# Kernel optimization log

Measured on AMD Instinct MI355X. Metric: run time of the kernel, lower is better.

## Reference

```python
import jax, jax.numpy as jnp
import numpy as np
from jax import lax

B = 32768  # number of 5x5 patches processed in a batch
NUM_MID = 6  # middle 25->25 conv layers (layers 1..6 of 8)
NUM_W = 6    # predicted kernel weights per pixel


def _conv(x, w, b, pad):
    # x: [B,C,H,W], w: [O,I,kh,kw]
    y = lax.conv_general_dilated(x, w, (1, 1), pad,
                                 dimension_numbers=('NCHW', 'OIHW', 'NCHW'))
    return y + b[None, :, None, None]


def setup_inputs() -> dict:
    key = jax.random.key(0)
    ks = jax.random.split(key, 10)
    s = 0.1
    inp = {
        'input': jax.random.normal(ks[0], (B, 8, 5, 5), dtype=jnp.float32),
        'w0': jax.random.normal(ks[1], (25, 8, 3, 3), dtype=jnp.float32) * s,
        'b0': jax.random.normal(ks[2], (25,), dtype=jnp.float32) * s,
        'wmid': jax.random.normal(ks[3], (NUM_MID, 25, 25, 3, 3), dtype=jnp.float32) * s,
        'bmid': jax.random.normal(ks[4], (NUM_MID, 25), dtype=jnp.float32) * s,
        'wlast': jax.random.normal(ks[5], (NUM_W, 25, 3, 3), dtype=jnp.float32) * s,
        'blast': jax.random.normal(ks[6], (NUM_W,), dtype=jnp.float32) * s,
        'wpost': jax.random.normal(ks[7], (3 * NUM_W, 3, 5, 5), dtype=jnp.float32) * s,
        'bpost': jax.random.normal(ks[8], (3 * NUM_W,), dtype=jnp.float32) * s,
    }
    return inp


def reference(input, w0, b0, wmid, bmid, wlast, blast, wpost, bpost):
    # 8-layer tiny CNN predicting per-pixel softmax weights over NUM_W kernels
    h = jax.nn.relu(_conv(input, w0, b0, 'SAME'))
    for i in range(NUM_MID):  # fixed small layer count
        h = jax.nn.relu(_conv(h, wmid[i], bmid[i], 'SAME'))
    h = _conv(h, wlast, blast, 'SAME')            # [B, NUM_W, 5, 5]
    norm_w = jax.nn.softmax(h, axis=1)            # softmax over weight channels
    # postconv: 5x5 valid conv on first 3 channels -> [B, 3*NUM_W, 1, 1] -> [B,3,NUM_W]
    colors = _conv(input[:, 0:3], wpost, bpost, 'VALID').reshape(B, 3, NUM_W)
    # per-pixel matmul: filtered[:,y,x] = colors @ norm_w[:,y,x]
    filtered = jnp.einsum('bcw,bwyx->bcyx', colors, norm_w)  # [B,3,5,5]
    return filtered
```

## Files before the change

kernel.cpp:

```cpp
#include <hip/hip_runtime.h>
#include <hip/hip_bf16.h>
#include <stdint.h>


typedef short bf16x8 __attribute__((ext_vector_type(8)));
typedef float f32x4  __attribute__((ext_vector_type(4)));

#define WSB_N     73728
#define WSB_EMB   6144
#define WSF_BYTE  147456
#define WSF_BALL  0
#define WSF_BP32  256
#define WSF_N     1624

__device__ __forceinline__ float b2f(unsigned short u) {
  union { unsigned int u; float f; } v; v.u = ((unsigned int)u) << 16; return v.f;
}
__device__ __forceinline__ unsigned short f2b(float f) {
  union { float f; unsigned int u; } v; v.f = f;
  unsigned int r = v.u + 0x7fffu + ((v.u >> 16) & 1u);
  return (unsigned short)(r >> 16);
}
__device__ __forceinline__ unsigned int pk2(float lo, float hi) {
  __hip_bfloat162 h = __float22bfloat162_rn(make_float2(lo, hi));
  union { __hip_bfloat162 h; unsigned int u; } v; v.h = h; return v.u;
}
__device__ __forceinline__ bool sniff_is_f32(const void* w0raw) {
  const unsigned short* q = (const unsigned short*)w0raw;
  int hits = 0;
  #pragma unroll
  for (int i = 0; i < 64; ++i) {
    unsigned int e = (q[i] >> 7) & 0xFFu;
    if (e >= 130u) ++hits;
  }
  return hits > 0;
}
__device__ __forceinline__ float ldw(const void* p, long idx, bool f32) {
  return f32 ? ((const float*)p)[idx] : b2f(((const unsigned short*)p)[idx]);
}
__device__ __forceinline__ int kperm(int m) {
  return (m < 16) ? ((m >> 2) * 8 + (m & 3))
                  : (((m - 16) >> 2) * 8 + 4 + (m & 3));
}

__global__ void prep_weights(const void* __restrict__ w0,
                             const void* __restrict__ b0,
                             const void* __restrict__ wm,
                             const void* __restrict__ bm,
                             const void* __restrict__ wl,
                             const void* __restrict__ bl,
                             const void* __restrict__ wp,
                             const void* __restrict__ bp,
                             unsigned short* __restrict__ wsb,
                             float* __restrict__ wsf) {
  const bool f32 = sniff_is_f32(w0);
  int e = blockIdx.x * blockDim.x + threadIdx.x;
  if (e < WSB_N) {
    int l = e / 9216, r = e % 9216, t = r / 1024, r2 = r % 1024;
    int o = r2 >> 5, c = r2 & 31;
    if (l == 7 && o >= 6) return;
    float v = 0.f;
    if (l < 7) {
      int co = kperm(o);
      if (co < 25) {
        if (l == 0) { if (c < 8)  v = ldw(w0, (co * 8 + c) * 9 + t, f32); }
        else        { if (c < 25) v = ldw(wm, (((l - 1) * 25 + co) * 25 + c) * 9 + t, f32); }
      }
    } else {
      if (c < 25) v = ldw(wl, (o * 25 + c) * 9 + t, f32);
    }
    wsb[e] = f2b(v);
  } else if (e < WSB_N + WSB_EMB) {
    int idx = e - WSB_N;
    int hl = idx / 3072, rem = idx % 3072;
    int chunk = rem / 1024, r2 = rem % 1024;
    int o = r2 >> 5, k = r2 & 31;
    float w = (o < 18 && k < 25) ? ldw(wp, (o * 3 + chunk) * 25 + k, f32) : 0.f;
    unsigned short hi = f2b(w);
    unsigned short val = hl ? f2b(w - b2f(hi)) : hi;
    int rowidx = hl * 96 + chunk * 32 + o;
    int t = rowidx / 26, rr = 6 + rowidx % 26;
    wsb[7 * 9216 + t * 1024 + rr * 32 + k] = val;
  } else {
    int q = e - WSB_N - WSB_EMB;
    if (q < 256) {
      int l = q >> 5, m = q & 31;
      float v = 0.f;
      if (l < 7) {
        int co = kperm(m);
        if (co < 25) v = (l == 0) ? ldw(b0, co, f32) : ldw(bm, (l - 1) * 25 + co, f32);
      } else {
        if (m < 6) v = ldw(bl, m, f32);
      }
      wsf[WSF_BALL + q] = v;
    } else if (q < 288) {
      int oc = q - 256;
      wsf[WSF_BP32 + oc] = (oc < 18) ? ldw(bp, oc, f32) : 0.f;
    }
  }
}

__global__ __launch_bounds__(64)
__attribute__((amdgpu_waves_per_eu(2, 2)))
void pcnn_mfma(
    const void* __restrict__ inp,
    const void* __restrict__ w0raw,
    const unsigned short* __restrict__ wsb,
    const float* __restrict__ wsf,
    void* __restrict__ out) {
  __shared__ __align__(16) unsigned char pool[13696];
  short* stage = (short*)pool;
  short* inpk  = (short*)(pool + 6400);
  float* colb  = (float*)(pool + 12544);
  float* smb   = (float*)pool;

  const bool f32m = sniff_is_f32(w0raw);
  const int lane = threadIdx.x;
  const int col  = lane & 15;
  const int quad = lane >> 4;
  const long g   = blockIdx.x;

  bf16x8 WC[2][3][2];
  #pragma unroll
  for (int hl = 0; hl < 2; ++hl)
    #pragma unroll
    for (int ch = 0; ch < 3; ++ch)
      #pragma unroll
      for (int hf = 0; hf < 2; ++hf) {
        const int rowidx = hl * 96 + ch * 32 + hf * 16 + col;
        const int t = rowidx / 26, rr = 6 + rowidx % 26;
        WC[hl][ch][hf] = *(const bf16x8*)(wsb + 7 * 9216 + t * 1024 + rr * 32 + quad * 8);
      }
  f32x4 c0 = *(const f32x4*)(wsf + WSF_BP32 + quad * 4);
  f32x4 c1 = *(const f32x4*)(wsf + WSF_BP32 + 16 + quad * 4);

  for (int i = lane; i < 672; i += 64) {
    int s = 25 + i % 7, rest = i / 7;
    inpk[rest * 32 + s] = 0;
  }

  #pragma unroll 1
  for (int c0i = 0; c0i < 3200; c0i += 1600) {
    float v[25];
    #pragma unroll
    for (int j = 0; j < 25; ++j)
      v[j] = ldw(inp, g * 3200 + c0i + j * 64 + lane, f32m);
    #pragma unroll
    for (int j = 0; j < 25; ++j) {
      const int e = c0i + j * 64 + lane;
      int b = e / 200, r = e % 200, c = r / 25, px = r % 25;
      unsigned short hi = f2b(v[j]);
      stage[px * 128 + b * 8 + c] = hi;
      if (c < 3) {
        inpk[((0 * 3 + c) * 16 + b) * 32 + px] = hi;
        inpk[((1 * 3 + c) * 16 + b) * 32 + px] = f2b(v[j] - b2f(hi));
      }
    }
  }
  __asm__ volatile("s_waitcnt lgkmcnt(0)" ::: "memory");

  #pragma unroll
  for (int ch = 0; ch < 3; ++ch) {
    bf16x8 Bhi = *(const bf16x8*)(inpk + ((0 * 3 + ch) * 16 + col) * 32 + quad * 8);
    bf16x8 Blo = *(const bf16x8*)(inpk + ((1 * 3 + ch) * 16 + col) * 32 + quad * 8);
    c0 = __builtin_amdgcn_mfma_f32_16x16x32_bf16(WC[0][ch][0], Bhi, c0, 0, 0, 0);
    c0 = __builtin_amdgcn_mfma_f32_16x16x32_bf16(WC[0][ch][0], Blo, c0, 0, 0, 0);
    c0 = __builtin_amdgcn_mfma_f32_16x16x32_bf16(WC[1][ch][0], Bhi, c0, 0, 0, 0);
    c1 = __builtin_amdgcn_mfma_f32_16x16x32_bf16(WC[0][ch][1], Bhi, c1, 0, 0, 0);
    c1 = __builtin_amdgcn_mfma_f32_16x16x32_bf16(WC[0][ch][1], Blo, c1, 0, 0, 0);
    c1 = __builtin_amdgcn_mfma_f32_16x16x32_bf16(WC[1][ch][1], Bhi, c1, 0, 0, 0);
  }
  #pragma unroll
  for (int r = 0; r < 4; ++r) colb[col * 18 + quad * 4 + r] = c0[r];
  if (quad == 0) { colb[col * 18 + 16] = c1[0]; colb[col * 18 + 17] = c1[1]; }

  bf16x8 X[25], Y[25];
  #pragma unroll
  for (int p = 0; p < 25; ++p) {
    union { bf16x8 v; uint4 q4; } t;
    t.q4 = make_uint4(0u, 0u, 0u, 0u);
    if (quad == 0) t.q4 = *(const uint4*)(stage + p * 128 + col * 8);
    X[p] = t.v;
  }

  auto conv = [&](const bf16x8 (&in)[25], bf16x8 (&outp)[25], int l) {
    const unsigned short* WA = wsb + l * 9216;
    bf16x8 A0[9], A1[9];
    #pragma unroll
    for (int t = 0; t < 9; ++t) {
      A0[t] = *(const bf16x8*)(WA + t * 1024 + col * 32 + quad * 8);
      A1[t] = *(const bf16x8*)(WA + t * 1024 + (16 + col) * 32 + quad * 8);
    }
    const f32x4 bias0 = *(const f32x4*)(wsf + WSF_BALL + l * 32 + quad * 4);
    const f32x4 bias1 = *(const f32x4*)(wsf + WSF_BALL + l * 32 + 16 + quad * 4);
    #pragma unroll
    for (int p = 0; p < 25; ++p) {
      const int py = p / 5, pxx = p % 5;
      f32x4 a0e = bias0, a1e = bias1;
      f32x4 a0o = {0.f, 0.f, 0.f, 0.f}, a1o = {0.f, 0.f, 0.f, 0.f};
      __builtin_amdgcn_s_setprio(1);
      #pragma unroll
      for (int dy = -1; dy <= 1; ++dy)
        #pragma unroll
        for (int dx = -1; dx <= 1; ++dx)
          if ((unsigned)(py + dy) < 5u && (unsigned)(pxx + dx) < 5u) {
            const int t = (dy + 1) * 3 + (dx + 1);
            const int q = p + dy * 5 + dx;
            if (t & 1) {
              a0o = __builtin_amdgcn_mfma_f32_16x16x32_bf16(A0[t], in[q], a0o, 0, 0, 0);
              a1o = __builtin_amdgcn_mfma_f32_16x16x32_bf16(A1[t], in[q], a1o, 0, 0, 0);
            } else {
              a0e = __builtin_amdgcn_mfma_f32_16x16x32_bf16(A0[t], in[q], a0e, 0, 0, 0);
              a1e = __builtin_amdgcn_mfma_f32_16x16x32_bf16(A1[t], in[q], a1e, 0, 0, 0);
            }
          }
      __builtin_amdgcn_s_setprio(0);
      union { bf16x8 v; unsigned int uu[4]; } nb;
      nb.uu[0] = pk2(fmaxf(a0e[0] + a0o[0], 0.f), fmaxf(a0e[1] + a0o[1], 0.f));
      nb.uu[1] = pk2(fmaxf(a0e[2] + a0o[2], 0.f), fmaxf(a0e[3] + a0o[3], 0.f));
      nb.uu[2] = pk2(fmaxf(a1e[0] + a1o[0], 0.f), fmaxf(a1e[1] + a1o[1], 0.f));
      nb.uu[3] = pk2(fmaxf(a1e[2] + a1o[2], 0.f), fmaxf(a1e[3] + a1o[3], 0.f));
      outp[p] = nb.v;
    }
  };

  conv(X, Y, 0);
  #pragma unroll 1
  for (int i = 0; i < 3; ++i) {
    conv(Y, X, 2 * i + 1);
    conv(X, Y, 2 * i + 2);
  }

  {
    const unsigned short* WA = wsb + 7 * 9216;
    bf16x8 A[9];
    #pragma unroll
    for (int t = 0; t < 9; ++t)
      A[t] = *(const bf16x8*)(WA + t * 1024 + col * 32 + quad * 8);
    const f32x4 biasl = *(const f32x4*)(wsf + WSF_BALL + 7 * 32 + quad * 4);
    #pragma unroll
    for (int p = 0; p < 25; ++p) {
      const int py = p / 5, pxx = p % 5;
      f32x4 ae = biasl, ao = {0.f, 0.f, 0.f, 0.f};
      __builtin_amdgcn_s_setprio(1);
      #pragma unroll
      for (int dy = -1; dy <= 1; ++dy)
        #pragma unroll
        for (int dx = -1; dx <= 1; ++dx)
          if ((unsigned)(py + dy) < 5u && (unsigned)(pxx + dx) < 5u) {
            const int t = (dy + 1) * 3 + (dx + 1);
            const int q = p + dy * 5 + dx;
            if (t & 1)
              ao = __builtin_amdgcn_mfma_f32_16x16x32_bf16(A[t], Y[q], ao, 0, 0, 0);
            else
              ae = __builtin_amdgcn_mfma_f32_16x16x32_bf16(A[t], Y[q], ae, 0, 0, 0);
          }
      __builtin_amdgcn_s_setprio(0);
      f32x4 a;
      a[0] = ae[0] + ao[0]; a[1] = ae[1] + ao[1];
      a[2] = ae[2] + ao[2]; a[3] = ae[3] + ao[3];
      float l4 = __shfl_xor(a[0], 16);
      float l5 = __shfl_xor(a[1], 16);
      if (quad == 0) {
        float m = fmaxf(fmaxf(fmaxf(a[0], a[1]), fmaxf(a[2], a[3])), fmaxf(l4, l5));
        float e0 = __expf(a[0] - m), e1 = __expf(a[1] - m), e2 = __expf(a[2] - m);
        float e3 = __expf(a[3] - m), e4 = __expf(l4 - m), e5 = __expf(l5 - m);
        float inv = 1.f / (e0 + e1 + e2 + e3 + e4 + e5);
        float* sp = smb + p * 96 + col * 6;
        sp[0] = e0 * inv; sp[1] = e1 * inv; sp[2] = e2 * inv;
        sp[3] = e3 * inv; sp[4] = e4 * inv; sp[5] = e5 * inv;
      }
    }
  }
  __asm__ volatile("s_waitcnt lgkmcnt(0)" ::: "memory");

  for (int e = lane; e < 1200; e += 64) {
    int b = e / 75, r = e % 75, c = r / 25, p = r % 25;
    float v = 0.f;
    #pragma unroll
    for (int w = 0; w < 6; ++w)
      v = fmaf(colb[b * 18 + c * 6 + w], smb[p * 96 + b * 6 + w], v);
    const long oidx = g * 1200 + e;
    if (f32m) ((float*)out)[oidx] = v;
    else      ((unsigned short*)out)[oidx] = f2b(v);
  }
}

extern "C" void kernel_launch(void* const* d_in, const int* in_sizes, int n_in,
                              void* d_out, int out_size, void* d_ws, size_t ws_size,
                              hipStream_t stream) {
  unsigned short* wsb = (unsigned short*)d_ws;
  float* wsf = (float*)((char*)d_ws + WSF_BYTE);
  const int B = in_sizes[0] / 200;

  const int prep_n = WSB_N + WSB_EMB + 288;
  prep_weights<<<(prep_n + 255) / 256, 256, 0, stream>>>(
      d_in[1], d_in[2], d_in[3], d_in[4], d_in[5], d_in[6], d_in[7], d_in[8],
      wsb, wsf);
  pcnn_mfma<<<B / 16, 64, 0, stream>>>(d_in[0], d_in[1], wsb, wsf, d_out);
}
```

Baseline: 159.4 us.

## Software-pipeline conv epilogues behind next pixel's MFMAs and pad LDS strides

The per-pixel epilogue (bias add, ReLU, bf16 pack, and in the last layer the softmax) is delayed by one iteration, so it runs while the next pixel's MFMA chain is in flight instead of stalling on the accumulator results. Separately, the LDS staging stride and the softmax buffer stride are padded (128 to 136 shorts, 96 to 98 floats) to reduce bank conflicts, and the shared pool grows to match. The cost is extra live accumulator registers, which could add pressure under the fixed waves-per-EU setting.

```diff
diff --git a/kernel.cpp b/kernel.cpp
--- a/kernel.cpp
+++ b/kernel.cpp
@@ -11,7 +11,12 @@
 #define WSF_BYTE  147456
 #define WSF_BALL  0
 #define WSF_BP32  256
-#define WSF_N     1624
+
+#define L_STAGE_STRIDE 136
+#define L_INPK   6800
+#define L_COLB   12944
+#define L_POOL   14096
+#define SMB_STRIDE 98
 
 __device__ __forceinline__ float b2f(unsigned short u) {
   union { unsigned int u; float f; } v; v.u = ((unsigned int)u) << 16; return v.f;
@@ -108,10 +113,10 @@
     const unsigned short* __restrict__ wsb,
     const float* __restrict__ wsf,
     void* __restrict__ out) {
-  __shared__ __align__(16) unsigned char pool[13696];
+  __shared__ __align__(16) unsigned char pool[L_POOL];
   short* stage = (short*)pool;
-  short* inpk  = (short*)(pool + 6400);
-  float* colb  = (float*)(pool + 12544);
+  short* inpk  = (short*)(pool + L_INPK);
+  float* colb  = (float*)(pool + L_COLB);
   float* smb   = (float*)pool;
 
   const bool f32m = sniff_is_f32(w0raw);
@@ -150,7 +155,7 @@
       const int e = c0i + j * 64 + lane;
       int b = e / 200, r = e % 200, c = r / 25, px = r % 25;
       unsigned short hi = f2b(v[j]);
-      stage[px * 128 + b * 8 + c] = hi;
+      stage[px * L_STAGE_STRIDE + b * 8 + c] = hi;
       if (c < 3) {
         inpk[((0 * 3 + c) * 16 + b) * 32 + px] = hi;
         inpk[((1 * 3 + c) * 16 + b) * 32 + px] = f2b(v[j] - b2f(hi));
@@ -179,7 +184,7 @@
   for (int p = 0; p < 25; ++p) {
     union { bf16x8 v; uint4 q4; } t;
     t.q4 = make_uint4(0u, 0u, 0u, 0u);
-    if (quad == 0) t.q4 = *(const uint4*)(stage + p * 128 + col * 8);
+    if (quad == 0) t.q4 = *(const uint4*)(stage + p * L_STAGE_STRIDE + col * 8);
     X[p] = t.v;
   }
 
@@ -193,6 +198,7 @@
     }
     const f32x4 bias0 = *(const f32x4*)(wsf + WSF_BALL + l * 32 + quad * 4);
     const f32x4 bias1 = *(const f32x4*)(wsf + WSF_BALL + l * 32 + 16 + quad * 4);
+    f32x4 p0e, p0o, p1e, p1o;
     #pragma unroll
     for (int p = 0; p < 25; ++p) {
       const int py = p / 5, pxx = p % 5;
@@ -215,12 +221,23 @@
             }
           }
       __builtin_amdgcn_s_setprio(0);
+      if (p > 0) {
+        union { bf16x8 v; unsigned int uu[4]; } nb;
+        nb.uu[0] = pk2(fmaxf(p0e[0] + p0o[0], 0.f), fmaxf(p0e[1] + p0o[1], 0.f));
+        nb.uu[1] = pk2(fmaxf(p0e[2] + p0o[2], 0.f), fmaxf(p0e[3] + p0o[3], 0.f));
+        nb.uu[2] = pk2(fmaxf(p1e[0] + p1o[0], 0.f), fmaxf(p1e[1] + p1o[1], 0.f));
+        nb.uu[3] = pk2(fmaxf(p1e[2] + p1o[2], 0.f), fmaxf(p1e[3] + p1o[3], 0.f));
+        outp[p - 1] = nb.v;
+      }
+      p0e = a0e; p0o = a0o; p1e = a1e; p1o = a1o;
+    }
+    {
       union { bf16x8 v; unsigned int uu[4]; } nb;
-      nb.uu[0] = pk2(fmaxf(a0e[0] + a0o[0], 0.f), fmaxf(a0e[1] + a0o[1], 0.f));
-      nb.uu[1] = pk2(fmaxf(a0e[2] + a0o[2], 0.f), fmaxf(a0e[3] + a0o[3], 0.f));
-      nb.uu[2] = pk2(fmaxf(a1e[0] + a1o[0], 0.f), fmaxf(a1e[1] + a1o[1], 0.f));
-      nb.uu[3] = pk2(fmaxf(a1e[2] + a1o[2], 0.f), fmaxf(a1e[3] + a1o[3], 0.f));
-      outp[p] = nb.v;
+      nb.uu[0] = pk2(fmaxf(p0e[0] + p0o[0], 0.f), fmaxf(p0e[1] + p0o[1], 0.f));
+      nb.uu[1] = pk2(fmaxf(p0e[2] + p0o[2], 0.f), fmaxf(p0e[3] + p0o[3], 0.f));
+      nb.uu[2] = pk2(fmaxf(p1e[0] + p1o[0], 0.f), fmaxf(p1e[1] + p1o[1], 0.f));
+      nb.uu[3] = pk2(fmaxf(p1e[2] + p1o[2], 0.f), fmaxf(p1e[3] + p1o[3], 0.f));
+      outp[24] = nb.v;
     }
   };
 
@@ -238,6 +255,20 @@
     for (int t = 0; t < 9; ++t)
       A[t] = *(const bf16x8*)(WA + t * 1024 + col * 32 + quad * 8);
     const f32x4 biasl = *(const f32x4*)(wsf + WSF_BALL + 7 * 32 + quad * 4);
+    f32x4 pa;
+    auto tail = [&](const f32x4& a, int p) {
+      float l4 = __shfl_xor(a[0], 16);
+      float l5 = __shfl_xor(a[1], 16);
+      if (quad == 0) {
+        float m = fmaxf(fmaxf(fmaxf(a[0], a[1]), fmaxf(a[2], a[3])), fmaxf(l4, l5));
+        float e0 = __expf(a[0] - m), e1 = __expf(a[1] - m), e2 = __expf(a[2] - m);
+        float e3 = __expf(a[3] - m), e4 = __expf(l4 - m), e5 = __expf(l5 - m);
+        float inv = 1.f / (e0 + e1 + e2 + e3 + e4 + e5);
+        float* sp = smb + p * SMB_STRIDE + col * 6;
+        sp[0] = e0 * inv; sp[1] = e1 * inv; sp[2] = e2 * inv;
+        sp[3] = e3 * inv; sp[4] = e4 * inv; sp[5] = e5 * inv;
+      }
+    };
     #pragma unroll
     for (int p = 0; p < 25; ++p) {
       const int py = p / 5, pxx = p % 5;
@@ -256,21 +287,13 @@
               ae = __builtin_amdgcn_mfma_f32_16x16x32_bf16(A[t], Y[q], ae, 0, 0, 0);
           }
       __builtin_amdgcn_s_setprio(0);
+      if (p > 0) tail(pa, p - 1);
       f32x4 a;
       a[0] = ae[0] + ao[0]; a[1] = ae[1] + ao[1];
       a[2] = ae[2] + ao[2]; a[3] = ae[3] + ao[3];
-      float l4 = __shfl_xor(a[0], 16);
-      float l5 = __shfl_xor(a[1], 16);
-      if (quad == 0) {
-        float m = fmaxf(fmaxf(fmaxf(a[0], a[1]), fmaxf(a[2], a[3])), fmaxf(l4, l5));
-        float e0 = __expf(a[0] - m), e1 = __expf(a[1] - m), e2 = __expf(a[2] - m);
-        float e3 = __expf(a[3] - m), e4 = __expf(l4 - m), e5 = __expf(l5 - m);
-        float inv = 1.f / (e0 + e1 + e2 + e3 + e4 + e5);
-        float* sp = smb + p * 96 + col * 6;
-        sp[0] = e0 * inv; sp[1] = e1 * inv; sp[2] = e2 * inv;
-        sp[3] = e3 * inv; sp[4] = e4 * inv; sp[5] = e5 * inv;
-      }
-    }
+      pa = a;
+    }
+    tail(pa, 24);
   }
   __asm__ volatile("s_waitcnt lgkmcnt(0)" ::: "memory");
 
@@ -279,7 +302,7 @@
     float v = 0.f;
     #pragma unroll
     for (int w = 0; w < 6; ++w)
-      v = fmaf(colb[b * 18 + c * 6 + w], smb[p * 96 + b * 6 + w], v);
+      v = fmaf(colb[b * 18 + c * 6 + w], smb[p * SMB_STRIDE + b * 6 + w], v);
     const long oidx = g * 1200 + e;
     if (f32m) ((float*)out)[oidx] = v;
     else      ((unsigned short*)out)[oidx] = f2b(v);
```

New measurement: 155.0 us. -2.7%, faster.
